# Kernel optimization log

Hardware: AMD Instinct MI355X
Metric: run time of the kernel (lower is better)

Reference implementation:

```python
import jax, jax.numpy as jnp
import numpy as np

B, C, T, V, D, H, KT = 64, 3, 256, 21, 128, 4, 9


def _adjacency():
    rng = np.random.default_rng(0)
    Araw = (rng.random((V, V)) < 0.3).astype(np.float32)
    Araw = np.maximum(Araw, Araw.T)
    np.fill_diagonal(Araw, 1.0)
    deg = Araw.sum(1)
    Anorm = Araw / np.sqrt(deg[:, None] * deg[None, :])  # D^-1/2 A D^-1/2
    return Araw.astype(np.float32), Anorm.astype(np.float32)


def setup_inputs() -> dict:
    key = jax.random.key(0)
    ks = jax.random.split(key, 24)
    g = lambda i, shape, sc=0.05: jax.random.normal(ks[i], shape, dtype=jnp.float32) * sc
    Araw, Anorm = _adjacency()
    return {
        'x': jax.random.normal(ks[0], (B, C, T, V), dtype=jnp.float32),
        'coord_w': g(1, (C, D)), 'coord_b': g(2, (D,)),
        'joint_emb': g(3, (V, D)),
        'graph_bias': jnp.asarray(Araw),  # nn.Parameter(A.clone().float())
        'wq': g(4, (D, D)), 'bq': g(5, (D,)),
        'wk': g(6, (D, D)), 'bk': g(7, (D,)),
        'wv': g(8, (D, D)), 'bv': g(9, (D,)),
        'wo': g(10, (D, D)), 'bo': g(11, (D,)),
        'gcn_w1': g(12, (D, D)), 'gcn_b1': g(13, (D,)),
        'tcn_w1': g(14, (D, D, KT, 1)), 'tcn_b1': g(15, (D,)),
        'gcn_w2': g(16, (D, D)), 'gcn_b2': g(17, (D,)),
        'tcn_w2': g(18, (D, D, KT, 1)), 'tcn_b2': g(19, (D,)),
        'A': jnp.asarray(Anorm),  # fixed normalized adjacency buffer
    }


def _stgcn(x, A, gw, gb, tw, tb):
    # x: [B, D, T, V]; spatial graph conv then temporal conv, residual.
    res = x
    y = jnp.einsum('bctv,vw->bctw', x, A)              # neighbor aggregation
    y = jnp.einsum('bctv,dc->bdtv', y, gw) + gb[None, :, None, None]
    y = jax.nn.relu(y)
    y = jax.lax.conv_general_dilated(
        y, tw, window_strides=(1, 1), padding=((KT // 2, KT // 2), (0, 0)),
        dimension_numbers=('NCHW', 'OIHW', 'NCHW'))     # temporal conv, kernel 9
    y = y + tb[None, :, None, None]
    return jax.nn.relu(y + res)


def reference(x, coord_w, coord_b, joint_emb, graph_bias, wq, bq, wk, bk, wv, bv,
              wo, bo, gcn_w1, gcn_b1, tcn_w1, tcn_b1, gcn_w2, gcn_b2, tcn_w2,
              tcn_b2, A):
    b, c, t, v = x.shape
    d = coord_w.shape[1]
    dh = d // H
    scale = jnp.float32(1.0 / np.sqrt(dh))
    coords = x.transpose(0, 2, 3, 1).reshape(b * t, v, c)      # [N, V, 3]
    feat = coords @ coord_w + coord_b + joint_emb              # LearnedJointEncoding
    q = (feat @ wq + bq).reshape(-1, v, H, dh)
    k = (feat @ wk + bk).reshape(-1, v, H, dh)
    val = (feat @ wv + bv).reshape(-1, v, H, dh)
    scores = jnp.einsum('nihd,njhd->nhij', q, k) * scale + graph_bias[None, None]
    attn = jax.nn.softmax(scores, axis=-1)                     # [N, H, V, V]
    out = jnp.einsum('nhij,njhd->nihd', attn, val).reshape(-1, v, d)
    feat = out @ wo + bo
    feat = feat.reshape(b, t, v, d).transpose(0, 3, 1, 2)       # [B, D, T, V]
    feat = _stgcn(feat, A, gcn_w1, gcn_b1, tcn_w1, tcn_b1)
    feat = _stgcn(feat, A, gcn_w2, gcn_b2, tcn_w2, tcn_b2)
    return feat, attn
```

## Files before the change

kernel.cpp:

```cpp
#include <hip/hip_runtime.h>
#include <hip/hip_bf16.h>

typedef __hip_bfloat16 bf16;
typedef __attribute__((ext_vector_type(8))) short short8v;
typedef __attribute__((ext_vector_type(4))) float float4v;

#define BB   64
#define CC   3
#define TLEN 256
#define VJ   21
#define DM   128
#define NH   4
#define DH   32
#define KT   9
#define NFR  (BB*TLEN)
#define MTOK (NFR*VJ)
#define NIN  22


__device__ __forceinline__ float b2f(bf16 x){ return __bfloat162float(x); }
__device__ __forceinline__ bf16  f2b(float x){ return __float2bfloat16(x); }
__device__ __forceinline__ float hb2f(short s){ return __uint_as_float(((unsigned)(unsigned short)s) << 16); }
__device__ __forceinline__ float lo16(unsigned u){ return __uint_as_float(u << 16); }
__device__ __forceinline__ float hi16(unsigned u){ return __uint_as_float(u & 0xffff0000u); }

__global__ void detect_dtype(const void* __restrict__ xin, int nus, int* __restrict__ flag){
  const unsigned short* u = (const unsigned short*)xin;
  int lim = nus < 65536 ? nus : 65536;
  int bad = 0;
  for (int k = threadIdx.x; k < lim; k += 256){
    float f = __uint_as_float(((unsigned)u[k]) << 16);
    if (!(fabsf(f) < 1e6f)) bad = 1;
  }
  if (bad) atomicOr(flag, 1);
}

struct ConvArgs { const void* src[NIN]; int off[NIN+1]; };

__global__ void convert_inputs(ConvArgs a, bf16* __restrict__ dst,
                               const int* __restrict__ flag, int total){
  int i = blockIdx.x*256 + threadIdx.x;
  if (i >= total) return;
  bool isf32 = (*flag != 0);
  int k = 0;
  while (i >= a.off[k+1]) ++k;
  int j = i - a.off[k];
  float v;
  if (isf32) v = ((const float*)a.src[k])[j];
  else       v = __uint_as_float(((unsigned)((const unsigned short*)a.src[k])[j]) << 16);
  dst[i] = f2b(v);
}

__global__ void prep_weights(const bf16* __restrict__ wq, const bf16* __restrict__ wk,
                             const bf16* __restrict__ wv, const bf16* __restrict__ wo,
                             const bf16* __restrict__ tw1, const bf16* __restrict__ tw2,
                             bf16* __restrict__ wqT, bf16* __restrict__ wkT,
                             bf16* __restrict__ wvT, bf16* __restrict__ woT,
                             bf16* __restrict__ twT1, bf16* __restrict__ twT2){
  int i = blockIdx.x*256 + threadIdx.x;
  if (i < DM*DM){
    int d = i >> 7, e = i & 127;
    wqT[i] = wq[e*DM + d];
    wkT[i] = wk[e*DM + d];
    wvT[i] = wv[e*DM + d];
    woT[i] = wo[e*DM + d];
  }
  if (i < KT*DM*DM){
    int c = i & 127; int d = (i >> 7) & 127; int tap = i >> 14;
    twT1[i] = tw1[(d*DM + c)*KT + tap];
    twT2[i] = tw2[(d*DM + c)*KT + tap];
  }
}

__global__ __launch_bounds__(512) void qkv_gemm(const bf16* __restrict__ x,
                                                const bf16* __restrict__ cw,
                                                const bf16* __restrict__ cb,
                                                const bf16* __restrict__ je,
                                                const bf16* __restrict__ BtQ,
                                                const bf16* __restrict__ BtK,
                                                const bf16* __restrict__ BtV,
                                                const bf16* __restrict__ bq,
                                                const bf16* __restrict__ bk,
                                                const bf16* __restrict__ bv,
                                                bf16* __restrict__ Oq,
                                                bf16* __restrict__ Ok,
                                                bf16* __restrict__ Ov){
  __shared__ short8v lds[128*16];
  __shared__ float sxf[128][4];
  const int tid = threadIdx.x;
  const int r0  = blockIdx.x*128;
  const int bvi = r0 >> 8;
  const int t0  = r0 & (TLEN-1);
  const int blk_b = bvi / VJ, blk_v = bvi % VJ;
  {
    int tok = tid >> 2, c = tid & 3;
    if (tok < 128 && c < 3)
      sxf[tok][c] = b2f(x[((size_t)(blk_b*CC + c)*TLEN + t0 + tok)*VJ + blk_v]);
  }
  __syncthreads();
  for (int i = tid; i < 128*16; i += 512){
    int row = i >> 4, c0 = i & 15;
    short8v cw0 = *reinterpret_cast<const short8v*>(cw + 0*DM + c0*8);
    short8v cw1 = *reinterpret_cast<const short8v*>(cw + 1*DM + c0*8);
    short8v cw2 = *reinterpret_cast<const short8v*>(cw + 2*DM + c0*8);
    short8v cbv = *reinterpret_cast<const short8v*>(cb + c0*8);
    short8v jev = *reinterpret_cast<const short8v*>(je + blk_v*DM + c0*8);
    float x0 = sxf[row][0], x1 = sxf[row][1], x2 = sxf[row][2];
    short8v out;
    #pragma unroll
    for (int e = 0; e < 8; ++e){
      float f = hb2f(cbv[e]) + hb2f(jev[e]);
      f = fmaf(x0, hb2f(cw0[e]), f);
      f = fmaf(x1, hb2f(cw1[e]), f);
      f = fmaf(x2, hb2f(cw2[e]), f);
      bf16 h = f2b(f);
      out[e] = *reinterpret_cast<short*>(&h);
    }
    lds[row*16 + (c0 ^ (row & 7))] = out;
  }
  __syncthreads();
  const int lane = tid & 63;
  const int wid  = tid >> 6;
  const int rbase = (wid >> 2) * 64;
  const int nt0   = (wid & 3) * 2;
  const int l15 = lane & 15, l4 = lane >> 4;
  #pragma unroll
  for (int w = 0; w < 3; ++w){
    const bf16* Bt  = (w==0) ? BtQ : (w==1) ? BtK : BtV;
    const bf16* bia = (w==0) ? bq  : (w==1) ? bk  : bv;
    bf16*       Out = (w==0) ? Oq  : (w==1) ? Ok  : Ov;
    short8v breg[2][4];
    #pragma unroll
    for (int ntl = 0; ntl < 2; ++ntl)
      #pragma unroll
      for (int ks = 0; ks < 4; ++ks)
        breg[ntl][ks] = *reinterpret_cast<const short8v*>(Bt + ((nt0+ntl)*16 + l15)*DM + ks*32 + l4*8);
    float4v acc[4][2];
    #pragma unroll
    for (int rt = 0; rt < 4; ++rt){ acc[rt][0] = (float4v){0,0,0,0}; acc[rt][1] = (float4v){0,0,0,0}; }
    #pragma unroll
    for (int rt = 0; rt < 4; ++rt){
      const int ldsRow = rbase + rt*16 + l15;
      #pragma unroll
      for (int ks = 0; ks < 4; ++ks){
        short8v a = lds[ldsRow*16 + ((ks*4 + l4) ^ (ldsRow & 7))];
        acc[rt][0] = __builtin_amdgcn_mfma_f32_16x16x32_bf16(a, breg[0][ks], acc[rt][0], 0,0,0);
        acc[rt][1] = __builtin_amdgcn_mfma_f32_16x16x32_bf16(a, breg[1][ks], acc[rt][1], 0,0,0);
      }
    }
    #pragma unroll
    for (int rt = 0; rt < 4; ++rt)
      #pragma unroll
      for (int ntl = 0; ntl < 2; ++ntl){
        int col = (nt0+ntl)*16 + l15;
        float bvv = b2f(bia[col]);
        #pragma unroll
        for (int j = 0; j < 4; ++j)
          Out[(size_t)(r0 + rbase + rt*16 + l4*4 + j)*DM + col] = f2b(acc[rt][ntl][j] + bvv);
      }
  }
}

template<int NTAPS, bool RELU, bool RESID>
__global__ __launch_bounds__(512, 4) void conv_gemm(const bf16* __restrict__ A,
                                                    const bf16* __restrict__ Bt,
                                                    const bf16* __restrict__ bias,
                                                    const bf16* resid,
                                                    bf16* Cout){
  constexpr int HT   = NTAPS/2;
  constexpr int ROWS = 128 + 2*HT;
  __shared__ short8v lds[ROWS*16];
  const int tid = threadIdx.x;
  const int r0  = blockIdx.x*128;
  const int t0  = r0 & (TLEN-1);
  const long mb = r0 - t0;
  for (int i = tid; i < ROWS*16; i += 512){
    int row = i >> 4, c0 = i & 15;
    int t = t0 + row - HT;
    if (t < 0) t = 0;
    if (t > TLEN-1) t = TLEN-1;
    lds[row*16 + (c0 ^ (row & 7))] = *reinterpret_cast<const short8v*>(A + (mb + t)*DM + c0*8);
  }
  __syncthreads();
  const int lane = tid & 63;
  const int wid  = tid >> 6;
  const int rbase = (wid >> 2) * 64;
  const int nt0   = (wid & 3) * 2;
  const int l15 = lane & 15, l4 = lane >> 4;
  float4v acc[4][2];
  #pragma unroll
  for (int rt = 0; rt < 4; ++rt){ acc[rt][0] = (float4v){0,0,0,0}; acc[rt][1] = (float4v){0,0,0,0}; }

  #pragma unroll
  for (int tap = 0; tap < NTAPS; ++tap){
    const bf16* Btap = Bt + (size_t)tap*DM*DM;
    short8v breg[2][4];
    #pragma unroll
    for (int ntl = 0; ntl < 2; ++ntl)
      #pragma unroll
      for (int ks = 0; ks < 4; ++ks)
        breg[ntl][ks] = *reinterpret_cast<const short8v*>(Btap + ((nt0+ntl)*16 + l15)*DM + ks*32 + l4*8);
    const int dt = tap - HT;
    #pragma unroll
    for (int rt = 0; rt < 4; ++rt){
      const int tl = rbase + rt*16 + l15;
      bool valid = true;
      if (NTAPS > 1){
        int ts = t0 + tl + dt;
        valid = (ts >= 0) && (ts < TLEN);
      }
      const int ldsRow = tl + HT + dt;
      #pragma unroll
      for (int ks = 0; ks < 4; ++ks){
        short8v a = lds[ldsRow*16 + ((ks*4 + l4) ^ (ldsRow & 7))];
        if (NTAPS > 1 && !valid) a = (short8v){0,0,0,0,0,0,0,0};
        acc[rt][0] = __builtin_amdgcn_mfma_f32_16x16x32_bf16(a, breg[0][ks], acc[rt][0], 0,0,0);
        acc[rt][1] = __builtin_amdgcn_mfma_f32_16x16x32_bf16(a, breg[1][ks], acc[rt][1], 0,0,0);
      }
    }
  }
  #pragma unroll
  for (int rt = 0; rt < 4; ++rt){
    #pragma unroll
    for (int ntl = 0; ntl < 2; ++ntl){
      int col = (nt0+ntl)*16 + l15;
      float bv = b2f(bias[col]);
      #pragma unroll
      for (int j = 0; j < 4; ++j){
        size_t idx = (size_t)(r0 + rbase + rt*16 + l4*4 + j)*DM + col;
        float val = acc[rt][ntl][j] + bv;
        if (RESID) val += b2f(resid[idx]);
        if (RELU) val = fmaxf(val, 0.f);
        Cout[idx] = f2b(val);
      }
    }
  }
}

__global__ __launch_bounds__(256) void attn_core(const bf16* __restrict__ Q,
                                                 const bf16* __restrict__ K,
                                                 const bf16* __restrict__ V,
                                                 const bf16* __restrict__ gbias,
                                                 const bf16* __restrict__ woT,
                                                 const bf16* __restrict__ bo,
                                                 float* __restrict__ attn_out,
                                                 bf16* __restrict__ feat_out){
  const int n = blockIdx.x;
  const int bb = n / TLEN, t = n % TLEN;
  const int tid = threadIdx.x;
  __shared__ bf16 skv[3][VJ][136];
  __shared__ float sc[NH*VJ*VJ];
  __shared__ float rmax[NH*VJ], rinv[NH*VJ];
  __shared__ bf16 sgb[VJ*VJ];
  __shared__ short8v sao[32*16];

  for (int i = tid; i < VJ*VJ; i += 256) sgb[i] = gbias[i];
  for (int i = tid; i < 3*VJ*16; i += 256){
    int c0 = i & 15; int v = (i >> 4) % VJ; int w = i / (16*VJ);
    size_t m = ((size_t)bb*VJ + v)*TLEN + t;
    const bf16* src = (w==0 ? Q : (w==1 ? K : V)) + m*DM + c0*8;
    *reinterpret_cast<short8v*>(&skv[w][v][c0*8]) = *reinterpret_cast<const short8v*>(src);
  }
  __syncthreads();
  const float scale = 0.17677669529663687f;
  for (int idx = tid; idx < NH*VJ*VJ; idx += 256){
    int j = idx % VJ, i2 = (idx/VJ) % VJ, h = idx/(VJ*VJ);
    const unsigned* qr = reinterpret_cast<const unsigned*>(&skv[0][i2][h*DH]);
    const unsigned* kr = reinterpret_cast<const unsigned*>(&skv[1][j][h*DH]);
    float a = 0.f;
    #pragma unroll
    for (int p = 0; p < DH/2; ++p){
      unsigned qa = qr[p], ka = kr[p];
      a = fmaf(lo16(qa), lo16(ka), a);
      a = fmaf(hi16(qa), hi16(ka), a);
    }
    sc[idx] = a*scale + b2f(sgb[i2*VJ + j]);
  }
  __syncthreads();
  for (int r = tid; r < NH*VJ; r += 256){
    float m = -1e30f;
    for (int j = 0; j < VJ; ++j) m = fmaxf(m, sc[r*VJ + j]);
    float s = 0.f;
    for (int j = 0; j < VJ; ++j) s += __expf(sc[r*VJ + j] - m);
    rmax[r] = m; rinv[r] = 1.0f/s;
  }
  __syncthreads();
  for (int idx = tid; idx < NH*VJ*VJ; idx += 256){
    int r = idx / VJ;
    float e = __expf(sc[idx] - rmax[r]) * rinv[r];
    sc[idx] = e;
    attn_out[(size_t)n*(NH*VJ*VJ) + idx] = e;
  }
  __syncthreads();
  for (int i = tid; i < VJ*(DM/2); i += 256){
    int q2 = i & 63; int v = i >> 6;
    int d0 = q2*2; int h = d0 >> 5;
    const float* pr = &sc[(h*VJ + v)*VJ];
    float a0 = 0.f, a1 = 0.f;
    #pragma unroll
    for (int j = 0; j < VJ; ++j){
      unsigned va = *reinterpret_cast<const unsigned*>(&skv[2][j][d0]);
      float p = pr[j];
      a0 = fmaf(p, lo16(va), a0);
      a1 = fmaf(p, hi16(va), a1);
    }
    bf16 b0 = f2b(a0), b1 = f2b(a1);
    unsigned u0 = *reinterpret_cast<unsigned short*>(&b0);
    unsigned u1 = *reinterpret_cast<unsigned short*>(&b1);
    unsigned* lp = reinterpret_cast<unsigned*>(&sao[v*16 + ((q2 >> 2) ^ (v & 7))]);
    lp[q2 & 3] = u0 | (u1 << 16);
  }
  __syncthreads();
  const int lane = tid & 63;
  const int wid  = tid >> 6;
  const int l15 = lane & 15, l4 = lane >> 4;
  float4v acc[2][2];
  #pragma unroll
  for (int mt = 0; mt < 2; ++mt){ acc[mt][0] = (float4v){0,0,0,0}; acc[mt][1] = (float4v){0,0,0,0}; }
  #pragma unroll
  for (int ks = 0; ks < 4; ++ks){
    short8v bfr[2];
    #pragma unroll
    for (int ct = 0; ct < 2; ++ct)
      bfr[ct] = *reinterpret_cast<const short8v*>(woT + (wid*32 + ct*16 + l15)*DM + ks*32 + l4*8);
    #pragma unroll
    for (int mt = 0; mt < 2; ++mt){
      int row = mt*16 + l15;
      short8v a = sao[row*16 + ((ks*4 + l4) ^ (row & 7))];
      acc[mt][0] = __builtin_amdgcn_mfma_f32_16x16x32_bf16(a, bfr[0], acc[mt][0], 0,0,0);
      acc[mt][1] = __builtin_amdgcn_mfma_f32_16x16x32_bf16(a, bfr[1], acc[mt][1], 0,0,0);
    }
  }
  #pragma unroll
  for (int mt = 0; mt < 2; ++mt){
    #pragma unroll
    for (int ct = 0; ct < 2; ++ct){
      int col = wid*32 + ct*16 + l15;
      float bov = b2f(bo[col]);
      #pragma unroll
      for (int j = 0; j < 4; ++j){
        int row = mt*16 + l4*4 + j;
        if (row < VJ)
          feat_out[(((size_t)bb*VJ + row)*TLEN + t)*DM + col] = f2b(acc[mt][ct][j] + bov);
      }
    }
  }
}

__global__ __launch_bounds__(256) void agg_kernel(const bf16* __restrict__ fin,
                                                  const bf16* __restrict__ An,
                                                  bf16* __restrict__ aout){
  const int n = blockIdx.x;
  const int bb = n / TLEN, t = n % TLEN;
  const int tid = threadIdx.x;
  __shared__ bf16 sx[VJ][136];
  __shared__ float sA[VJ*VJ];
  for (int i = tid; i < VJ*VJ; i += 256) sA[i] = b2f(An[i]);
  for (int i = tid; i < VJ*16; i += 256){
    int c0 = i & 15, v = i >> 4;
    size_t m = ((size_t)bb*VJ + v)*TLEN + t;
    *reinterpret_cast<short8v*>(&sx[v][c0*8]) =
      *reinterpret_cast<const short8v*>(fin + m*DM + c0*8);
  }
  __syncthreads();
  for (int i = tid; i < VJ*16; i += 256){
    int c0 = i & 15, w = i >> 4;
    float acc[8] = {0,0,0,0,0,0,0,0};
    #pragma unroll
    for (int u = 0; u < VJ; ++u){
      float a = sA[u*VJ + w];
      short8v xv = *reinterpret_cast<const short8v*>(&sx[u][c0*8]);
      #pragma unroll
      for (int e = 0; e < 8; ++e) acc[e] = fmaf(a, hb2f(xv[e]), acc[e]);
    }
    short8v out;
    #pragma unroll
    for (int e = 0; e < 8; ++e){ bf16 h = f2b(acc[e]); out[e] = *reinterpret_cast<short*>(&h); }
    size_t m = ((size_t)bb*VJ + w)*TLEN + t;
    *reinterpret_cast<short8v*>(aout + m*DM + c0*8) = out;
  }
}

__global__ __launch_bounds__(256) void transpose_out(const bf16* __restrict__ fin,
                                                     float* __restrict__ fout){
  const int bid = blockIdx.x;
  const int b   = bid >> 5;
  const int rem = bid & 31;
  const int t0  = (rem >> 2) * 32;
  const int d0  = (rem & 3) * 32;
  __shared__ bf16 tile[32][VJ][33];
  const int tid = threadIdx.x;
  for (int idx = tid; idx < 32*VJ*32; idx += 256){
    int dl = idx & 31;
    int v  = (idx >> 5) % VJ;
    int tl = idx / (32*VJ);
    tile[tl][v][dl] = fin[(((size_t)b*VJ + v)*TLEN + t0 + tl)*DM + d0 + dl];
  }
  __syncthreads();
  for (int idx = tid; idx < 32*VJ*32; idx += 256){
    int j  = idx % (32*VJ);
    int dl = idx / (32*VJ);
    int tl = j / VJ, v = j % VJ;
    fout[((size_t)(b*DM + d0 + dl)*TLEN + t0 + tl)*VJ + v] = b2f(tile[tl][v][dl]);
  }
}

extern "C" void kernel_launch(void* const* d_in, const int* in_sizes, int n_in,
                              void* d_out, int out_size, void* d_ws, size_t ws_size,
                              hipStream_t stream){
  const size_t featElems = (size_t)MTOK*DM;
  float* outf    = (float*)d_out;
  float* attnOut = outf + featElems;
  bf16* qbuf = (bf16*)d_out;
  bf16* kbuf = qbuf + featElems;

  char* wp = (char*)d_ws;
  auto alloc = [&](size_t bytes)->char*{ char* p = wp; wp += (bytes + 15) & ~(size_t)15; return p; };
  int*  flag = (int*)alloc(16);
  ConvArgs ca; int total = 0;
  for (int i = 0; i < NIN; ++i){ ca.src[i] = d_in[i]; ca.off[i] = total; total += in_sizes[i]; }
  ca.off[NIN] = total;
  bf16* cin   = (bf16*)alloc((size_t)total*2);
  bf16* wqT   = (bf16*)alloc(DM*DM*2);
  bf16* wkT   = (bf16*)alloc(DM*DM*2);
  bf16* wvT   = (bf16*)alloc(DM*DM*2);
  bf16* woT   = (bf16*)alloc(DM*DM*2);
  bf16* twT1  = (bf16*)alloc(KT*DM*DM*2);
  bf16* twT2  = (bf16*)alloc(KT*DM*DM*2);
  bf16* featA = (bf16*)alloc(featElems*2);
  bf16* bufV  = (bf16*)alloc(featElems*2);
  if ((size_t)(wp - (char*)d_ws) > ws_size) return;

  const bf16* x    = cin + ca.off[0];
  const bf16* cw   = cin + ca.off[1];
  const bf16* cb   = cin + ca.off[2];
  const bf16* je   = cin + ca.off[3];
  const bf16* gbias= cin + ca.off[4];
  const bf16* wq   = cin + ca.off[5];
  const bf16* bq   = cin + ca.off[6];
  const bf16* wk   = cin + ca.off[7];
  const bf16* bk   = cin + ca.off[8];
  const bf16* wv   = cin + ca.off[9];
  const bf16* bv   = cin + ca.off[10];
  const bf16* wo   = cin + ca.off[11];
  const bf16* bo   = cin + ca.off[12];
  const bf16* gw1  = cin + ca.off[13];
  const bf16* gb1  = cin + ca.off[14];
  const bf16* tw1  = cin + ca.off[15];
  const bf16* tb1  = cin + ca.off[16];
  const bf16* gw2  = cin + ca.off[17];
  const bf16* gb2  = cin + ca.off[18];
  const bf16* tw2  = cin + ca.off[19];
  const bf16* tb2  = cin + ca.off[20];
  const bf16* An   = cin + ca.off[21];

  const int GB = MTOK/128;
  hipMemsetAsync(flag, 0, sizeof(int), stream);
  detect_dtype<<<1, 256, 0, stream>>>(d_in[0], in_sizes[0], flag);
  convert_inputs<<<(total + 255)/256, 256, 0, stream>>>(ca, cin, flag, total);
  prep_weights<<<(KT*DM*DM + 255)/256, 256, 0, stream>>>(wq, wk, wv, wo, tw1, tw2,
                                                         wqT, wkT, wvT, woT, twT1, twT2);
  qkv_gemm<<<GB, 512, 0, stream>>>(x, cw, cb, je, wqT, wkT, wvT, bq, bk, bv,
                                   qbuf, kbuf, bufV);
  attn_core<<<NFR, 256, 0, stream>>>(qbuf, kbuf, bufV, gbias, woT, bo, attnOut, featA);
  agg_kernel<<<NFR, 256, 0, stream>>>(featA, An, qbuf);
  conv_gemm<1,true,false><<<GB, 512, 0, stream>>>(qbuf, gw1, gb1, nullptr, kbuf);
  conv_gemm<9,true,true><<<GB, 512, 0, stream>>>(kbuf, twT1, tb1, featA, featA);
  agg_kernel<<<NFR, 256, 0, stream>>>(featA, An, qbuf);
  conv_gemm<1,true,false><<<GB, 512, 0, stream>>>(qbuf, gw2, gb2, nullptr, kbuf);
  conv_gemm<9,true,true><<<GB, 512, 0, stream>>>(kbuf, twT2, tb2, featA, featA);
  transpose_out<<<BB*(TLEN/32)*(DM/32), 256, 0, stream>>>(featA, outf);
}
```

Before: 1.271 ms.

## Fuse GCN pointwise GEMM into temporal conv kernel via LDS intermediate

Replaces the separate 1x1 GCN GEMM and 9-tap temporal conv kernels with one kernel. Each block computes the GCN projection with bias and ReLU for its 128 rows plus an 8-row halo into shared memory, zeroing out-of-range time steps, then runs the temporal conv from that tile. This removes writing and re-reading the intermediate activation through global memory. In exchange it recomputes halo rows and streams GCN weights from global per job.

Measured after the change: 1.398 ms. +10.0%, slower.

```diff
diff --git a/kernel.cpp b/kernel.cpp
--- a/kernel.cpp
+++ b/kernel.cpp
@@ -16,6 +16,8 @@
 #define NFR  (BB*TLEN)
 #define MTOK (NFR*VJ)
 #define NIN  22
+#define HROW 8
+#define RWS  (128 + 2*HROW)
 
 
 __device__ __forceinline__ float b2f(bf16 x){ return __bfloat162float(x); }
@@ -161,59 +163,80 @@
   }
 }
 
-template<int NTAPS, bool RELU, bool RESID>
-__global__ __launch_bounds__(512, 4) void conv_gemm(const bf16* __restrict__ A,
-                                                    const bf16* __restrict__ Bt,
-                                                    const bf16* __restrict__ bias,
+__global__ __launch_bounds__(512, 4) void gcn_tconv(const bf16* __restrict__ Ain,
+                                                    const bf16* __restrict__ gw,
+                                                    const bf16* __restrict__ gb,
+                                                    const bf16* __restrict__ twT,
+                                                    const bf16* __restrict__ tb,
                                                     const bf16* resid,
                                                     bf16* Cout){
-  constexpr int HT   = NTAPS/2;
-  constexpr int ROWS = 128 + 2*HT;
-  __shared__ short8v lds[ROWS*16];
+  __shared__ short8v ldsA[RWS*16];
+  __shared__ short8v ldsB[RWS*16];
   const int tid = threadIdx.x;
   const int r0  = blockIdx.x*128;
   const int t0  = r0 & (TLEN-1);
   const long mb = r0 - t0;
-  for (int i = tid; i < ROWS*16; i += 512){
+  for (int i = tid; i < RWS*16; i += 512){
     int row = i >> 4, c0 = i & 15;
-    int t = t0 + row - HT;
-    if (t < 0) t = 0;
-    if (t > TLEN-1) t = TLEN-1;
-    lds[row*16 + (c0 ^ (row & 7))] = *reinterpret_cast<const short8v*>(A + (mb + t)*DM + c0*8);
+    int t = t0 + row - HROW;
+    int tc = t < 0 ? 0 : (t > TLEN-1 ? TLEN-1 : t);
+    ldsA[row*16 + (c0 ^ (row & 7))] = *reinterpret_cast<const short8v*>(Ain + (mb + tc)*DM + c0*8);
   }
   __syncthreads();
   const int lane = tid & 63;
   const int wid  = tid >> 6;
+  const int l15 = lane & 15, l4 = lane >> 4;
+  bf16* pB = reinterpret_cast<bf16*>(ldsB);
+  for (int job = wid; job < 18; job += 8){
+    int rt9 = job >> 1, ch = job & 1;
+    int arow = rt9*16 + l15;
+    float4v acc1[4];
+    #pragma unroll
+    for (int ct = 0; ct < 4; ++ct) acc1[ct] = (float4v){0,0,0,0};
+    #pragma unroll
+    for (int ks = 0; ks < 4; ++ks){
+      short8v a = ldsA[arow*16 + ((ks*4 + l4) ^ (arow & 7))];
+      #pragma unroll
+      for (int ct = 0; ct < 4; ++ct){
+        short8v b = *reinterpret_cast<const short8v*>(gw + (ch*64 + ct*16 + l15)*DM + ks*32 + l4*8);
+        acc1[ct] = __builtin_amdgcn_mfma_f32_16x16x32_bf16(a, b, acc1[ct], 0,0,0);
+      }
+    }
+    #pragma unroll
+    for (int ct = 0; ct < 4; ++ct){
+      int col = ch*64 + ct*16 + l15;
+      float gbv = b2f(gb[col]);
+      #pragma unroll
+      for (int j = 0; j < 4; ++j){
+        int row = rt9*16 + l4*4 + j;
+        int t = t0 + row - HROW;
+        float val = (t >= 0 && t < TLEN) ? fmaxf(acc1[ct][j] + gbv, 0.f) : 0.f;
+        pB[row*128 + ((((col >> 3) ^ (row & 7)) << 3) | (col & 7))] = f2b(val);
+      }
+    }
+  }
+  __syncthreads();
   const int rbase = (wid >> 2) * 64;
   const int nt0   = (wid & 3) * 2;
-  const int l15 = lane & 15, l4 = lane >> 4;
   float4v acc[4][2];
   #pragma unroll
   for (int rt = 0; rt < 4; ++rt){ acc[rt][0] = (float4v){0,0,0,0}; acc[rt][1] = (float4v){0,0,0,0}; }
-
-  #pragma unroll
-  for (int tap = 0; tap < NTAPS; ++tap){
-    const bf16* Btap = Bt + (size_t)tap*DM*DM;
+  #pragma unroll
+  for (int tap = 0; tap < KT; ++tap){
+    const bf16* Btap = twT + (size_t)tap*DM*DM;
     short8v breg[2][4];
     #pragma unroll
     for (int ntl = 0; ntl < 2; ++ntl)
       #pragma unroll
       for (int ks = 0; ks < 4; ++ks)
         breg[ntl][ks] = *reinterpret_cast<const short8v*>(Btap + ((nt0+ntl)*16 + l15)*DM + ks*32 + l4*8);
-    const int dt = tap - HT;
+    const int dt = tap - KT/2;
     #pragma unroll
     for (int rt = 0; rt < 4; ++rt){
-      const int tl = rbase + rt*16 + l15;
-      bool valid = true;
-      if (NTAPS > 1){
-        int ts = t0 + tl + dt;
-        valid = (ts >= 0) && (ts < TLEN);
-      }
-      const int ldsRow = tl + HT + dt;
+      const int ldsRow = rbase + rt*16 + l15 + HROW + dt;
       #pragma unroll
       for (int ks = 0; ks < 4; ++ks){
-        short8v a = lds[ldsRow*16 + ((ks*4 + l4) ^ (ldsRow & 7))];
-        if (NTAPS > 1 && !valid) a = (short8v){0,0,0,0,0,0,0,0};
+        short8v a = ldsB[ldsRow*16 + ((ks*4 + l4) ^ (ldsRow & 7))];
         acc[rt][0] = __builtin_amdgcn_mfma_f32_16x16x32_bf16(a, breg[0][ks], acc[rt][0], 0,0,0);
         acc[rt][1] = __builtin_amdgcn_mfma_f32_16x16x32_bf16(a, breg[1][ks], acc[rt][1], 0,0,0);
       }
@@ -224,14 +247,12 @@
     #pragma unroll
     for (int ntl = 0; ntl < 2; ++ntl){
       int col = (nt0+ntl)*16 + l15;
-      float bv = b2f(bias[col]);
+      float bv = b2f(tb[col]);
       #pragma unroll
       for (int j = 0; j < 4; ++j){
         size_t idx = (size_t)(r0 + rbase + rt*16 + l4*4 + j)*DM + col;
-        float val = acc[rt][ntl][j] + bv;
-        if (RESID) val += b2f(resid[idx]);
-        if (RELU) val = fmaxf(val, 0.f);
-        Cout[idx] = f2b(val);
+        float val = acc[rt][ntl][j] + bv + b2f(resid[idx]);
+        Cout[idx] = f2b(fmaxf(val, 0.f));
       }
     }
   }
@@ -464,10 +485,8 @@
                                    qbuf, kbuf, bufV);
   attn_core<<<NFR, 256, 0, stream>>>(qbuf, kbuf, bufV, gbias, woT, bo, attnOut, featA);
   agg_kernel<<<NFR, 256, 0, stream>>>(featA, An, qbuf);
-  conv_gemm<1,true,false><<<GB, 512, 0, stream>>>(qbuf, gw1, gb1, nullptr, kbuf);
-  conv_gemm<9,true,true><<<GB, 512, 0, stream>>>(kbuf, twT1, tb1, featA, featA);
+  gcn_tconv<<<GB, 512, 0, stream>>>(qbuf, gw1, gb1, twT1, tb1, featA, featA);
   agg_kernel<<<NFR, 256, 0, stream>>>(featA, An, qbuf);
-  conv_gemm<1,true,false><<<GB, 512, 0, stream>>>(qbuf, gw2, gb2, nullptr, kbuf);
-  conv_gemm<9,true,true><<<GB, 512, 0, stream>>>(kbuf, twT2, tb2, featA, featA);
+  gcn_tconv<<<GB, 512, 0, stream>>>(qbuf, gw2, gb2, twT2, tb2, featA, featA);
   transpose_out<<<BB*(TLEN/32)*(DM/32), 256, 0, stream>>>(featA, outf);
 }
```
